# Optimization experiments

Hardware: AMD Instinct MI355X
Metric: run time of the kernel (lower is better)

## Reference

```python
import jax, jax.numpy as jnp
import numpy as np

D = 128      # d_model
H = 8        # n_heads
HD = D // H  # head_dim = 16
E = 256      # n_experts
R = 32       # kv_lora_rank
B, T = 4, 512
EPS = 1e-6


def _dense_init(k, fi, fo):
    s = float(1.0 / np.sqrt(fi))
    return jax.random.uniform(k, (fi, fo), minval=-s, maxval=s, dtype=jnp.float32)


def setup_inputs() -> dict:
    key = jax.random.key(0)
    ks = jax.random.split(key, 16)
    rng = np.random.RandomState(42)
    Q, _ = np.linalg.qr(rng.randn(D, D))
    glim = float(np.sqrt(6.0 / (D + D)))
    return {
        'x': jax.random.normal(ks[0], (B, T, D), dtype=jnp.float32),
        'g1': jnp.ones((D,), jnp.float32),
        'qW': _dense_init(ks[1], D, D), 'qb': jnp.zeros((D,), jnp.float32),
        'kdW': _dense_init(ks[2], D, R), 'kdb': jnp.zeros((R,), jnp.float32),
        'kuW': _dense_init(ks[3], R, 2 * D), 'kub': jnp.zeros((2 * D,), jnp.float32),
        'oW': _dense_init(ks[4], D, D), 'ob': jnp.zeros((D,), jnp.float32),
        'rot': jnp.asarray(Q, jnp.float32),
        'tq_scale': jnp.ones((D,), jnp.float32),
        's1W': _dense_init(ks[5], D, D), 's1b': jnp.zeros((D,), jnp.float32),
        's2W': _dense_init(ks[6], D, D), 's2b': jnp.zeros((D,), jnp.float32),
        'g2': jnp.ones((D,), jnp.float32),
        'gateW': _dense_init(ks[7], D, E), 'gateb': jnp.zeros((E,), jnp.float32),
        'expW': jax.random.uniform(ks[8], (E, D, D), minval=-glim, maxval=glim, dtype=jnp.float32),
        'm1W': _dense_init(ks[9], D, D), 'm1b': jnp.zeros((D,), jnp.float32),
        'm2W': _dense_init(ks[10], D, D), 'm2b': jnp.zeros((D,), jnp.float32),
    }


def _rmsnorm(x, g):
    return g * (x / jnp.sqrt(jnp.mean(x * x, axis=-1, keepdims=True) + EPS))


def _swiglu(x, w1, b1, w2, b2):
    gate = x @ w1 + b1
    return gate * jax.nn.sigmoid(gate) * (x @ w2 + b2)


def _mla(x, qW, qb, kdW, kdb, kuW, kub, oW, ob):
    b, t = x.shape[0], x.shape[1]
    q = (x @ qW + qb).reshape(b, t, H, HD)
    kv = ((x @ kdW + kdb) @ kuW + kub).reshape(b, t, H, 2 * HD)
    k, v = jnp.split(kv, 2, axis=-1)
    q = jax.nn.elu(q) + 1.0
    k = jax.nn.elu(k) + 1.0
    # linear attention: context[b,h,d,e] = sum_t k[b,t,h,d] v[b,t,h,e]
    context = jnp.einsum('bthd,bthe->bhde', k, v)
    out = jnp.einsum('bthd,bhde->bthe', q, context)
    k_sum = jnp.sum(k, axis=1)  # [b,h,d]
    z = 1.0 / (jnp.einsum('bthd,bhd->bth', q, k_sum) + EPS)
    out = out * z[..., None]
    return out.reshape(b, t, D) @ oW + ob


def _turbo_quant(x, rot, scale):
    x = x @ rot
    mag = jnp.sqrt(jnp.mean(x * x, axis=-1, keepdims=True) + EPS)
    phase = x / mag
    qp = jnp.clip(phase * 127.0, -127.0, 127.0) / 127.0
    phase = jax.lax.stop_gradient(qp - phase) + phase  # straight-through
    return phase * mag * scale


def _moe(h, gateW, gateb, expW, m1W, m1b, m2W, m2b):
    gate_scores = jax.nn.softmax(h @ gateW + gateb, axis=-1)  # [B,T,E]
    top_vals, top_idx = jax.lax.top_k(gate_scores, 2)
    top_w = top_vals / (jnp.sum(top_vals, axis=-1, keepdims=True) + EPS)
    # dense all-expert compute as in the original module
    eo = jnp.einsum('btd,edo->bteo', h, expW)  # [B,T,E,D]
    mask = jnp.sum(jax.nn.one_hot(top_idx, E, dtype=h.dtype) * top_w[..., None], axis=2)  # [B,T,E]
    wavg = jnp.einsum('bteo,bte->bto', eo, mask)
    wavg = _swiglu(wavg, m1W, m1b, m2W, m2b)
    diff_sq = jnp.square(eo - wavg[:, :, None, :])
    wvar = jnp.einsum('bteo,bte->bto', diff_sq, mask)
    consensus = jnp.exp(-jnp.mean(wvar, axis=-1))  # [B,T]
    return wavg, consensus


def reference(x, g1, qW, qb, kdW, kdb, kuW, kub, oW, ob, rot, tq_scale,
              s1W, s1b, s2W, s2b, g2, gateW, gateb, expW, m1W, m1b, m2W, m2b):
    attn_out = _turbo_quant(_mla(_rmsnorm(x, g1), qW, qb, kdW, kdb, kuW, kub, oW, ob), rot, tq_scale)
    x = x + _swiglu(attn_out, s1W, s1b, s2W, s2b)
    moe_out, consensus = _moe(_rmsnorm(x, g2), gateW, gateb, expW, m1W, m1b, m2W, m2b)
    return x + moe_out, consensus
```

## Files before the change

### kernel.cpp

```cpp
#include <hip/hip_runtime.h>
#include <math.h>

static constexpr int Dd    = 128;
static constexpr int NH    = 8;
static constexpr int NE    = 256;
static constexpr int RR    = 32;
static constexpr int TT    = 512;
static constexpr int NTOK  = 2048;
static constexpr int SLOTS = 256;
#define EPSF 1e-6f

static constexpr int FK_KV    = 0;
static constexpr int FD_CTX   = 4;
static constexpr int FD_OR    = 8;
static constexpr int FD_ROUTE = 9;
static constexpr int FD_EXP   = 10;
static constexpr int NFLAGS   = 266;

__device__ __forceinline__ float elu1(float v) { return v > 0.f ? v + 1.f : expf(v); }
__device__ __forceinline__ float sigm(float v) { return 1.f / (1.f + expf(-v)); }

__device__ __forceinline__ void flag_add(int* p) {
  __hip_atomic_fetch_add(p, 1, __ATOMIC_RELEASE, __HIP_MEMORY_SCOPE_AGENT);
}
__device__ __forceinline__ void flag_wait(int* p, int tgt) {
  int c = 0;
  while (__hip_atomic_load(p, __ATOMIC_ACQUIRE, __HIP_MEMORY_SCOPE_AGENT) < tgt) {
    __builtin_amdgcn_s_sleep(2);
    if (++c > (1 << 27)) break;
  }
}

struct AParams {
  const float *x, *g1, *qW, *qb, *kdW, *kdb, *kuW, *kub, *oW, *ob, *rot, *tqs;
  const float *s1W, *s1b, *s2W, *s2b, *g2, *gateW, *gateb, *expW;
  const float *m1W, *m1b, *m2W, *m2b;
  float *kvbuf, *ctx, *ksum, *oR, *bR, *h2buf, *ybuf, *out;
  int *cnt, *slottok, *flags;
};

__global__ __launch_bounds__(512, 4) void k_all(AParams P) {
  const int tid = threadIdx.x;
  const int bid = blockIdx.x;
  const int j = tid & 127, g = tid >> 7;
  const int lane = tid & 63;
  const int n0 = bid * 4;
  const int b = bid >> 7;

  __shared__ float sh[64 * 32];
  __shared__ float4 bufA[128], bufB[128];
  __shared__ float4 part[3][128];
  __shared__ float4 gpart[256];
  __shared__ float4 rtmp[2];
  __shared__ float wvS[4][4]; __shared__ int wiS[4][4];
  __shared__ float zS[4][4];
  __shared__ int sE[4][2]; __shared__ int sSlot[4][2]; __shared__ float sWt[4][2];
  __shared__ __align__(16) float hT[128 * 20];
  __shared__ float4 y1T[128], y2T[128], inT[128], sT[128];

  float4* kpart4 = (float4*)hT;
  float4* kdT4   = (float4*)(hT + 1024);

  float xres[4];
  {
    float v[4];
    if (tid < 128) {
#pragma unroll
      for (int t = 0; t < 4; t++) { xres[t] = P.x[(n0 + t) * Dd + j]; v[t] = xres[t] * xres[t]; }
#pragma unroll
      for (int o = 32; o > 0; o >>= 1) {
#pragma unroll
        for (int t = 0; t < 4; t++) v[t] += __shfl_xor(v[t], o, 64);
      }
      if (lane == 0) rtmp[tid >> 6] = make_float4(v[0], v[1], v[2], v[3]);
    }
  }
  __syncthreads();
  if (tid < 128) {
    float g1j = P.g1[j];
#pragma unroll
    for (int t = 0; t < 4; t++) {
      float ss = ((const float*)&rtmp[0])[t] + ((const float*)&rtmp[1])[t];
      ((float*)&bufB[j])[t] = g1j * xres[t] * rsqrtf(ss * (1.f / 128.f) + EPSF);
    }
  }
  __syncthreads();

  {
    float a0 = 0, a1 = 0, a2 = 0, a3 = 0;
    const float* Wp = P.qW + (g * 32) * Dd + j;
#pragma unroll 16
    for (int i = 0; i < 32; i++) {
      float4 h4 = bufB[g * 32 + i];
      float w = Wp[i * Dd];
      a0 += h4.x * w; a1 += h4.y * w; a2 += h4.z * w; a3 += h4.w * w;
    }
    if (g) part[g - 1][j] = make_float4(a0, a1, a2, a3);
    __syncthreads();
    if (g == 0) {
      float4 p0 = part[0][j], p1 = part[1][j], p2 = part[2][j];
      float bb = P.qb[j];
      ((float*)&bufA[j])[0] = elu1(a0 + p0.x + p1.x + p2.x + bb);
      ((float*)&bufA[j])[1] = elu1(a1 + p0.y + p1.y + p2.y + bb);
      ((float*)&bufA[j])[2] = elu1(a2 + p0.z + p1.z + p2.z + bb);
      ((float*)&bufA[j])[3] = elu1(a3 + p0.w + p1.w + p2.w + bb);
    }
    __syncthreads();
  }

  if (tid < 256) {
    int col = tid & 31, ksp = tid >> 5;
    float a0 = 0, a1 = 0, a2 = 0, a3 = 0;
    const float* Wp = P.kdW + (ksp * 16) * RR + col;
#pragma unroll
    for (int i = 0; i < 16; i++) {
      float4 h4 = bufB[ksp * 16 + i];
      float w = Wp[i * RR];
      a0 += h4.x * w; a1 += h4.y * w; a2 += h4.z * w; a3 += h4.w * w;
    }
    kpart4[ksp * 32 + col] = make_float4(a0, a1, a2, a3);
  }
  __syncthreads();
  if (tid < 32) {
    float bb = P.kdb[tid];
    float s0 = bb, s1 = bb, s2 = bb, s3 = bb;
#pragma unroll
    for (int k = 0; k < 8; k++) {
      float4 p = kpart4[k * 32 + tid];
      s0 += p.x; s1 += p.y; s2 += p.z; s3 += p.w;
    }
    kdT4[tid] = make_float4(s0, s1, s2, s3);
  }
  __syncthreads();

  {
    int col = tid & 255, kh = tid >> 8;
    float a0 = 0, a1 = 0, a2 = 0, a3 = 0;
    const float* Wp = P.kuW + (kh * 16) * 256 + col;
#pragma unroll
    for (int r = 0; r < 16; r++) {
      float4 k4 = kdT4[kh * 16 + r];
      float w = Wp[r * 256];
      a0 += k4.x * w; a1 += k4.y * w; a2 += k4.z * w; a3 += k4.w * w;
    }
    if (kh) gpart[col] = make_float4(a0, a1, a2, a3);
    __syncthreads();
    if (!kh) {
      float4 p = gpart[col];
      float bb = P.kub[col];
      bool isk = (col & 31) < 16;
      float v0 = a0 + p.x + bb, v1 = a1 + p.y + bb, v2 = a2 + p.z + bb, v3 = a3 + p.w + bb;
      P.kvbuf[(n0 + 0) * 256 + col] = isk ? elu1(v0) : v0;
      P.kvbuf[(n0 + 1) * 256 + col] = isk ? elu1(v1) : v1;
      P.kvbuf[(n0 + 2) * 256 + col] = isk ? elu1(v2) : v2;
      P.kvbuf[(n0 + 3) * 256 + col] = isk ? elu1(v3) : v3;
    }
  }
  __threadfence();
  __syncthreads();
  if (tid == 0) flag_add(&P.flags[FK_KV + b]);

  if (bid < 32) {
    int idx = bid * 512 + tid;
    int row = idx >> 7, col = idx & 127;
    const float* ow = P.oW + row * 128;
    float acc = 0.f;
#pragma unroll 8
    for (int k = 0; k < 128; k++) acc += ow[k] * P.rot[k * 128 + col];
    P.oR[idx] = acc;
    __threadfence();
    __syncthreads();
    if (tid == 0) flag_add(&P.flags[FD_OR]);
  } else if (bid == 32) {
    if (tid < 128) {
      float acc = 0.f;
#pragma unroll 8
      for (int k = 0; k < 128; k++) acc += P.ob[k] * P.rot[k * 128 + tid];
      P.bR[tid] = acc;
    }
    __threadfence();
    __syncthreads();
    if (tid == 0) flag_add(&P.flags[FD_OR]);
  }

  if (bid < 32) {
    const int bh = bid, bb = bh >> 3, h = bh & 7;
    if (tid == 0) flag_wait(&P.flags[FK_KV + bb], 128);
    __syncthreads();
    __threadfence();
    float acc = 0.f, ks = 0.f;
    const int d = tid >> 4, e = tid & 15;
    for (int c = 0; c < 8; c++) {
      __syncthreads();
#pragma unroll
      for (int r = 0; r < 4; r++) {
        int lin = r * 512 + tid;
        int tok = lin >> 5, off = lin & 31;
        sh[lin] = P.kvbuf[((bb * TT + c * 64 + tok) * 256) + h * 32 + off];
      }
      __syncthreads();
      if (tid < 256) {
#pragma unroll 4
        for (int t = 0; t < 64; t++) {
          float kk = sh[t * 32 + d];
          acc += kk * sh[t * 32 + 16 + e];
          ks += kk;
        }
      }
    }
    if (tid < 256) {
      P.ctx[bh * 256 + d * 16 + e] = acc;
      if (e == 0) P.ksum[bh * 16 + d] = ks;
    }
    __threadfence();
    __syncthreads();
    if (tid == 0) flag_add(&P.flags[FD_CTX + bb]);
  }

  if (tid == 0) flag_wait(&P.flags[FD_CTX + b], 8);
  if (tid == 1) flag_wait(&P.flags[FD_OR], 33);
  __syncthreads();
  __threadfence();

  if (tid < 128) {
    int h = j >> 4, e = j & 15;
    const float* cpt = P.ctx + (b * NH + h) * 256;
    const float* kpt = P.ksum + (b * NH + h) * 16;
    float num[4] = {0, 0, 0, 0}, den[4] = {0, 0, 0, 0};
#pragma unroll
    for (int d = 0; d < 16; d++) {
      float cx = cpt[d * 16 + e], ks = kpt[d];
      float4 q4 = bufA[h * 16 + d];
      num[0] += q4.x * cx; num[1] += q4.y * cx; num[2] += q4.z * cx; num[3] += q4.w * cx;
      den[0] += q4.x * ks; den[1] += q4.y * ks; den[2] += q4.z * ks; den[3] += q4.w * ks;
    }
#pragma unroll
    for (int t = 0; t < 4; t++) ((float*)&bufB[j])[t] = num[t] / (den[t] + EPSF);
  }
  __syncthreads();

  {
    float a0 = 0, a1 = 0, a2 = 0, a3 = 0;
    const float* Wp = P.oR + (g * 32) * Dd + j;
#pragma unroll 16
    for (int i = 0; i < 32; i++) {
      float4 h4 = bufB[g * 32 + i];
      float w = Wp[i * Dd];
      a0 += h4.x * w; a1 += h4.y * w; a2 += h4.z * w; a3 += h4.w * w;
    }
    if (g) part[g - 1][j] = make_float4(a0, a1, a2, a3);
    __syncthreads();
    float tot[4];
    if (g == 0) {
      float4 p0 = part[0][j], p1 = part[1][j], p2 = part[2][j];
      float bb = P.bR[j];
      tot[0] = a0 + p0.x + p1.x + p2.x + bb; tot[1] = a1 + p0.y + p1.y + p2.y + bb;
      tot[2] = a2 + p0.z + p1.z + p2.z + bb; tot[3] = a3 + p0.w + p1.w + p2.w + bb;
      float v[4];
#pragma unroll
      for (int t = 0; t < 4; t++) v[t] = tot[t] * tot[t];
#pragma unroll
      for (int o = 32; o > 0; o >>= 1) {
#pragma unroll
        for (int t = 0; t < 4; t++) v[t] += __shfl_xor(v[t], o, 64);
      }
      if (lane == 0) rtmp[tid >> 6] = make_float4(v[0], v[1], v[2], v[3]);
    }
    __syncthreads();
    if (g == 0) {
      float scj = P.tqs[j];
#pragma unroll
      for (int t = 0; t < 4; t++) {
        float ss = ((const float*)&rtmp[0])[t] + ((const float*)&rtmp[1])[t];
        float mag = sqrtf(ss * (1.f / 128.f) + EPSF);
        float zc = fminf(fmaxf(tot[t], -mag), mag);
        ((float*)&bufA[j])[t] = zc * scj;
      }
    }
    __syncthreads();
  }

  float xn[4] = {0.f, 0.f, 0.f, 0.f};
  {
    float a0 = 0, a1 = 0, a2 = 0, a3 = 0;
    const float* Wp = (g < 2 ? P.s1W : P.s2W) + ((g & 1) * 64) * Dd + j;
#pragma unroll 16
    for (int i = 0; i < 64; i++) {
      float4 h4 = bufA[(g & 1) * 64 + i];
      float w = Wp[i * Dd];
      a0 += h4.x * w; a1 += h4.y * w; a2 += h4.z * w; a3 += h4.w * w;
    }
    if (g) part[g - 1][j] = make_float4(a0, a1, a2, a3);
    __syncthreads();
    if (g == 0) {
      float b1 = P.s1b[j], b2 = P.s2b[j];
      float4 p0 = part[0][j], p1 = part[1][j], p2 = part[2][j];
      float gv[4], uv[4], v[4];
      gv[0] = a0 + p0.x + b1; gv[1] = a1 + p0.y + b1;
      gv[2] = a2 + p0.z + b1; gv[3] = a3 + p0.w + b1;
      uv[0] = p1.x + p2.x + b2; uv[1] = p1.y + p2.y + b2;
      uv[2] = p1.z + p2.z + b2; uv[3] = p1.w + p2.w + b2;
      float g2j = P.g2[j];
#pragma unroll
      for (int t = 0; t < 4; t++) {
        xn[t] = xres[t] + gv[t] * sigm(gv[t]) * uv[t];
        ((float*)&bufB[j])[t] = g2j * xn[t];
        v[t] = xn[t] * xn[t];
      }
#pragma unroll
      for (int o = 32; o > 0; o >>= 1) {
#pragma unroll
        for (int t = 0; t < 4; t++) v[t] += __shfl_xor(v[t], o, 64);
      }
      if (lane == 0) rtmp[tid >> 6] = make_float4(v[0], v[1], v[2], v[3]);
    }
    __syncthreads();
  }

  float val[4]; float r2v[4];
  {
    int col = tid & 255, kh = tid >> 8;
    float a0 = 0, a1 = 0, a2 = 0, a3 = 0;
    const float* Wp = P.gateW + (kh * 64) * NE + col;
#pragma unroll 16
    for (int i = 0; i < 64; i++) {
      float4 h4 = bufB[kh * 64 + i];
      float w = Wp[i * NE];
      a0 += h4.x * w; a1 += h4.y * w; a2 += h4.z * w; a3 += h4.w * w;
    }
    if (kh) gpart[col] = make_float4(a0, a1, a2, a3);
    __syncthreads();
#pragma unroll
    for (int t = 0; t < 4; t++) {
      float ss = ((const float*)&rtmp[0])[t] + ((const float*)&rtmp[1])[t];
      r2v[t] = rsqrtf(ss * (1.f / 128.f) + EPSF);
    }
    if (!kh) {
      float4 p = gpart[col];
      float bb = P.gateb[col];
      val[0] = (a0 + p.x) * r2v[0] + bb; val[1] = (a1 + p.y) * r2v[1] + bb;
      val[2] = (a2 + p.z) * r2v[2] + bb; val[3] = (a3 + p.w) * r2v[3] + bb;
    }
    if (tid < 128) {
#pragma unroll
      for (int t = 0; t < 4; t++)
        P.h2buf[(n0 + t) * Dd + j] = ((const float*)&bufB[j])[t] * r2v[t];
    }
  }
  __syncthreads();

  float m1[4]; int i1[4];
  {
    if (tid < 256) {
      float bv[4]; int bi[4];
#pragma unroll
      for (int t = 0; t < 4; t++) { bv[t] = val[t]; bi[t] = tid; }
#pragma unroll
      for (int o = 32; o > 0; o >>= 1) {
#pragma unroll
        for (int t = 0; t < 4; t++) {
          float wv = __shfl_xor(bv[t], o, 64);
          int wi = __shfl_xor(bi[t], o, 64);
          if (wv > bv[t] || (wv == bv[t] && wi < bi[t])) { bv[t] = wv; bi[t] = wi; }
        }
      }
      if (lane == 0) {
#pragma unroll
        for (int t = 0; t < 4; t++) { wvS[tid >> 6][t] = bv[t]; wiS[tid >> 6][t] = bi[t]; }
      }
    }
    __syncthreads();
    if (tid < 256) {
#pragma unroll
      for (int t = 0; t < 4; t++) {
        m1[t] = wvS[0][t]; i1[t] = wiS[0][t];
#pragma unroll
        for (int w = 1; w < 4; w++) {
          float cv = wvS[w][t]; int ci = wiS[w][t];
          if (cv > m1[t] || (cv == m1[t] && ci < i1[t])) { m1[t] = cv; i1[t] = ci; }
        }
      }
    }
    __syncthreads();
  }
  float m2[4]; int i2[4];
  {
    if (tid < 256) {
      float bv[4]; int bi[4];
#pragma unroll
      for (int t = 0; t < 4; t++) {
        bv[t] = (tid == i1[t]) ? -INFINITY : val[t];
        bi[t] = tid;
      }
#pragma unroll
      for (int o = 32; o > 0; o >>= 1) {
#pragma unroll
        for (int t = 0; t < 4; t++) {
          float wv = __shfl_xor(bv[t], o, 64);
          int wi = __shfl_xor(bi[t], o, 64);
          if (wv > bv[t] || (wv == bv[t] && wi < bi[t])) { bv[t] = wv; bi[t] = wi; }
        }
      }
      if (lane == 0) {
#pragma unroll
        for (int t = 0; t < 4; t++) { wvS[tid >> 6][t] = bv[t]; wiS[tid >> 6][t] = bi[t]; }
      }
    }
    __syncthreads();
    if (tid < 256) {
#pragma unroll
      for (int t = 0; t < 4; t++) {
        m2[t] = wvS[0][t]; i2[t] = wiS[0][t];
#pragma unroll
        for (int w = 1; w < 4; w++) {
          float cv = wvS[w][t]; int ci = wiS[w][t];
          if (cv > m2[t] || (cv == m2[t] && ci < i2[t])) { m2[t] = cv; i2[t] = ci; }
        }
      }
    }
    __syncthreads();
  }
  {
    if (tid < 256) {
      float v[4];
#pragma unroll
      for (int t = 0; t < 4; t++) v[t] = expf(val[t] - m1[t]);
#pragma unroll
      for (int o = 32; o > 0; o >>= 1) {
#pragma unroll
        for (int t = 0; t < 4; t++) v[t] += __shfl_xor(v[t], o, 64);
      }
      if (lane == 0) {
#pragma unroll
        for (int t = 0; t < 4; t++) zS[tid >> 6][t] = v[t];
      }
    }
    __syncthreads();
  }
  if (tid < 4) {
    int t = tid, tok = n0 + t;
    float Z = zS[0][t] + zS[1][t] + zS[2][t] + zS[3][t];
    float p1 = 1.f / Z;
    float p2 = expf(m2[t] - m1[t]) / Z;
    float s = p1 + p2 + EPSF;
    int e1 = i1[t], e2 = i2[t];
    int s1 = atomicAdd(&P.cnt[e1], 1); if (s1 > SLOTS - 1) s1 = SLOTS - 1;
    int s2 = atomicAdd(&P.cnt[e2], 1); if (s2 > SLOTS - 1) s2 = SLOTS - 1;
    int sl1 = e1 * SLOTS + s1, sl2 = e2 * SLOTS + s2;
    P.slottok[sl1] = tok; P.slottok[sl2] = tok;
    sE[t][0] = e1; sE[t][1] = e2;
    sSlot[t][0] = sl1; sSlot[t][1] = sl2;
    sWt[t][0] = p1 / s; sWt[t][1] = p2 / s;
  }

  __threadfence();
  __syncthreads();
  if (tid == 0) {
    flag_add(&P.flags[FD_ROUTE]);
    flag_wait(&P.flags[FD_ROUTE], 512);
  }
  __syncthreads();
  __threadfence();

  {
    const int e = bid >> 1, sub = bid & 1;
    int n = __hip_atomic_load(&P.cnt[e], __ATOMIC_RELAXED, __HIP_MEMORY_SCOPE_AGENT);
    if (n > SLOTS) n = SLOTS;
    const int base = e * SLOTS;
    const float* Wp = P.expW + (size_t)e * Dd * Dd + j;
    for (int t0 = sub * 16; t0 < n; t0 += 32) {
      int m = n - t0; if (m > 16) m = 16;
      __syncthreads();
      for (int tt = g; tt < m; tt += 4) {
        int tok = P.slottok[base + t0 + tt];
        hT[j * 20 + tt] = P.h2buf[tok * Dd + j];
      }
      __syncthreads();
      float acc[4] = {0, 0, 0, 0};
#pragma unroll 8
      for (int i = 0; i < 128; i++) {
        float w = Wp[i * Dd];
        float4 h4 = *(const float4*)&hT[i * 20 + g * 4];
        acc[0] += h4.x * w; acc[1] += h4.y * w; acc[2] += h4.z * w; acc[3] += h4.w * w;
      }
#pragma unroll
      for (int k = 0; k < 4; k++) {
        int tt = g * 4 + k;
        if (tt < m) P.ybuf[(size_t)(base + t0 + tt) * Dd + j] = acc[k];
      }
    }
    __threadfence();
    __syncthreads();
    if (tid == 0) flag_add(&P.flags[FD_EXP + e]);
  }

  if (tid < 8) {
    int t = tid >> 1, sl = tid & 1;
    flag_wait(&P.flags[FD_EXP + sE[t][sl]], 2);
  }
  __syncthreads();
  __threadfence();

  {
    float y1 = P.ybuf[(size_t)sSlot[g][0] * Dd + j];
    float y2 = P.ybuf[(size_t)sSlot[g][1] * Dd + j];
    ((float*)&y1T[j])[g] = y1;
    ((float*)&y2T[j])[g] = y2;
    ((float*)&inT[j])[g] = sWt[g][0] * y1 + sWt[g][1] * y2;
  }
  __syncthreads();

  {
    float a0 = 0, a1 = 0, a2 = 0, a3 = 0;
    const float* Wp = (g < 2 ? P.m1W : P.m2W) + ((g & 1) * 64) * Dd + j;
#pragma unroll 16
    for (int i = 0; i < 64; i++) {
      float4 h4 = inT[(g & 1) * 64 + i];
      float w = Wp[i * Dd];
      a0 += h4.x * w; a1 += h4.y * w; a2 += h4.z * w; a3 += h4.w * w;
    }
    if (g) part[g - 1][j] = make_float4(a0, a1, a2, a3);
    __syncthreads();
    if (g == 0) {
      float b1 = P.m1b[j], b2 = P.m2b[j];
      float4 p0 = part[0][j], p1 = part[1][j], p2 = part[2][j];
      float gv[4], uv[4];
      gv[0] = a0 + p0.x + b1; gv[1] = a1 + p0.y + b1;
      gv[2] = a2 + p0.z + b1; gv[3] = a3 + p0.w + b1;
      uv[0] = p1.x + p2.x + b2; uv[1] = p1.y + p2.y + b2;
      uv[2] = p1.z + p2.z + b2; uv[3] = p1.w + p2.w + b2;
#pragma unroll
      for (int t = 0; t < 4; t++) {
        float sv = gv[t] * sigm(gv[t]) * uv[t];
        ((float*)&sT[j])[t] = sv;
        P.out[(n0 + t) * Dd + j] = xn[t] + sv;
      }
    }
    __syncthreads();
  }

  if (tid < 128) {
    float v[4];
#pragma unroll
    for (int t = 0; t < 4; t++) {
      float sv = ((const float*)&sT[j])[t];
      float d1 = ((const float*)&y1T[j])[t] - sv;
      float d2 = ((const float*)&y2T[j])[t] - sv;
      v[t] = sWt[t][0] * d1 * d1 + sWt[t][1] * d2 * d2;
    }
#pragma unroll
    for (int o = 32; o > 0; o >>= 1) {
#pragma unroll
      for (int t = 0; t < 4; t++) v[t] += __shfl_xor(v[t], o, 64);
    }
    if (lane == 0) rtmp[tid >> 6] = make_float4(v[0], v[1], v[2], v[3]);
  }
  __syncthreads();
  if (tid < 4) {
    float s = ((const float*)&rtmp[0])[tid] + ((const float*)&rtmp[1])[tid];
    P.out[NTOK * Dd + n0 + tid] = expf(-s * (1.f / 128.f));
  }
}

__global__ __launch_bounds__(512) void k_pre_fb(
    const float* __restrict__ x, const float* __restrict__ g1,
    const float* __restrict__ qW, const float* __restrict__ qb,
    const float* __restrict__ kdW, const float* __restrict__ kdb,
    const float* __restrict__ kuW, const float* __restrict__ kub,
    const float* __restrict__ oW, const float* __restrict__ ob,
    const float* __restrict__ rot,
    float* __restrict__ qbuf, float* __restrict__ kvbuf,
    float* __restrict__ ctx, float* __restrict__ ksum,
    int* __restrict__ cnt,
    float* __restrict__ oR, float* __restrict__ bR) {
  const int tid = threadIdx.x;
  const int bid = blockIdx.x;
  const int j = tid & 127, g = tid >> 7;
  const int lane = tid & 63;
  const int n0 = bid * 4;

  __shared__ float4 h1T[128];
  __shared__ float4 part[3][128];
  __shared__ float4 kpart[8][32];
  __shared__ float4 kdT[32];
  __shared__ float4 kupart[256];
  __shared__ float4 rtmp[2];

  if (bid == 0) {
    for (int i = tid; i < 32 * 256; i += 512) ctx[i] = 0.f;
    ksum[tid] = 0.f;
    if (tid < NE) cnt[tid] = 0;
  }

  float xv[4];
  if (tid < 128) {
    float v[4];
#pragma unroll
    for (int t = 0; t < 4; t++) { xv[t] = x[(n0 + t) * Dd + j]; v[t] = xv[t] * xv[t]; }
#pragma unroll
    for (int o = 32; o > 0; o >>= 1) {
#pragma unroll
      for (int t = 0; t < 4; t++) v[t] += __shfl_xor(v[t], o, 64);
    }
    if (lane == 0) rtmp[tid >> 6] = make_float4(v[0], v[1], v[2], v[3]);
  }
  __syncthreads();
  if (tid < 128) {
    float g1j = g1[j];
#pragma unroll
    for (int t = 0; t < 4; t++) {
      float ss = ((const float*)&rtmp[0])[t] + ((const float*)&rtmp[1])[t];
      ((float*)&h1T[j])[t] = g1j * xv[t] * rsqrtf(ss * (1.f / 128.f) + EPSF);
    }
  }
  __syncthreads();

  {
    float a0 = 0, a1 = 0, a2 = 0, a3 = 0;
    const float* Wp = qW + (g * 32) * Dd + j;
#pragma unroll 16
    for (int i = 0; i < 32; i++) {
      float4 h4 = h1T[g * 32 + i];
      float w = Wp[i * Dd];
      a0 += h4.x * w; a1 += h4.y * w; a2 += h4.z * w; a3 += h4.w * w;
    }
    if (g) part[g - 1][j] = make_float4(a0, a1, a2, a3);
    __syncthreads();
    if (g == 0) {
      float4 p0 = part[0][j], p1 = part[1][j], p2 = part[2][j];
      float bb = qb[j];
      qbuf[(n0 + 0) * Dd + j] = elu1(a0 + p0.x + p1.x + p2.x + bb);
      qbuf[(n0 + 1) * Dd + j] = elu1(a1 + p0.y + p1.y + p2.y + bb);
      qbuf[(n0 + 2) * Dd + j] = elu1(a2 + p0.z + p1.z + p2.z + bb);
      qbuf[(n0 + 3) * Dd + j] = elu1(a3 + p0.w + p1.w + p2.w + bb);
    }
    __syncthreads();
  }

  if (tid < 256) {
    int col = tid & 31, ksp = tid >> 5;
    float a0 = 0, a1 = 0, a2 = 0, a3 = 0;
    const float* Wp = kdW + (ksp * 16) * RR + col;
#pragma unroll
    for (int i = 0; i < 16; i++) {
      float4 h4 = h1T[ksp * 16 + i];
      float w = Wp[i * RR];
      a0 += h4.x * w; a1 += h4.y * w; a2 += h4.z * w; a3 += h4.w * w;
    }
    kpart[ksp][col] = make_float4(a0, a1, a2, a3);
  }
  __syncthreads();
  if (tid < 32) {
    float bb = kdb[tid];
    float s0 = bb, s1 = bb, s2 = bb, s3 = bb;
#pragma unroll
    for (int k = 0; k < 8; k++) {
      float4 p = kpart[k][tid];
      s0 += p.x; s1 += p.y; s2 += p.z; s3 += p.w;
    }
    kdT[tid] = make_float4(s0, s1, s2, s3);
  }
  __syncthreads();

  {
    int col = tid & 255, kh = tid >> 8;
    float a0 = 0, a1 = 0, a2 = 0, a3 = 0;
    const float* Wp = kuW + (kh * 16) * 256 + col;
#pragma unroll
    for (int r = 0; r < 16; r++) {
      float4 k4 = kdT[kh * 16 + r];
      float w = Wp[r * 256];
      a0 += k4.x * w; a1 += k4.y * w; a2 += k4.z * w; a3 += k4.w * w;
    }
    if (kh) kupart[col] = make_float4(a0, a1, a2, a3);
    __syncthreads();
    if (!kh) {
      float4 p = kupart[col];
      float bb = kub[col];
      bool isk = (col & 31) < 16;
      float v0 = a0 + p.x + bb, v1 = a1 + p.y + bb, v2 = a2 + p.z + bb, v3 = a3 + p.w + bb;
      kvbuf[(n0 + 0) * 256 + col] = isk ? elu1(v0) : v0;
      kvbuf[(n0 + 1) * 256 + col] = isk ? elu1(v1) : v1;
      kvbuf[(n0 + 2) * 256 + col] = isk ? elu1(v2) : v2;
      kvbuf[(n0 + 3) * 256 + col] = isk ? elu1(v3) : v3;
    }
  }

  if (bid < 32) {
    int idx = bid * 512 + tid;
    int row = idx >> 7, col = idx & 127;
    const float* ow = oW + row * 128;
    float acc = 0.f;
#pragma unroll 8
    for (int k = 0; k < 128; k++) acc += ow[k] * rot[k * 128 + col];
    oR[idx] = acc;
  } else if (bid == 32 && tid < 128) {
    float acc = 0.f;
#pragma unroll 8
    for (int k = 0; k < 128; k++) acc += ob[k] * rot[k * 128 + tid];
    bR[tid] = acc;
  }
}

__global__ __launch_bounds__(256) void k_ctx_fb(const float* __restrict__ kv,
                                                float* __restrict__ ctx,
                                                float* __restrict__ ksum) {
  const int blk = blockIdx.x;
  const int tid = threadIdx.x;
  const int bh = blk >> 3, c = blk & 7;
  const int b = bh >> 3, h = bh & 7;
  const int d = tid >> 4, e = tid & 15;
  __shared__ float sh[64 * 32];
#pragma unroll
  for (int r = 0; r < 8; r++) {
    int lin = r * 256 + tid;
    int tok = lin >> 5, off = lin & 31;
    sh[lin] = kv[((b * TT + c * 64 + tok) * 256) + h * 32 + off];
  }
  __syncthreads();
  float acc = 0.f, ks = 0.f;
#pragma unroll 4
  for (int t = 0; t < 64; t++) {
    float kk = sh[t * 32 + d];
    acc += kk * sh[t * 32 + 16 + e];
    ks += kk;
  }
  atomicAdd(&ctx[bh * 256 + d * 16 + e], acc);
  if (e == 0) atomicAdd(&ksum[bh * 16 + d], ks);
}

__global__ __launch_bounds__(512) void k_mid_fb(
    const float* __restrict__ x, const float* __restrict__ qbuf,
    const float* __restrict__ ctx, const float* __restrict__ ksum,
    const float* __restrict__ oR, const float* __restrict__ bR,
    const float* __restrict__ tqs,
    const float* __restrict__ s1W, const float* __restrict__ s1b,
    const float* __restrict__ s2W, const float* __restrict__ s2b,
    const float* __restrict__ g2, const float* __restrict__ gateW,
    const float* __restrict__ gateb,
    float* __restrict__ xnbuf, float* __restrict__ h2buf,
    float* __restrict__ gw, int* __restrict__ tokslot,
    int* __restrict__ slottok, int* __restrict__ cnt) {
  const int tid = threadIdx.x;
  const int j = tid & 127, g = tid >> 7;
  const int lane = tid & 63;
  const int n0 = blockIdx.x * 4;
  const int b = n0 >> 9;

  __shared__ float4 bufA[128], bufB[128];
  __shared__ float4 part[3][128];
  __shared__ float4 gpart[256];
  __shared__ float4 rtmp[2];
  __shared__ float wvS[4][4]; __shared__ int wiS[4][4];
  __shared__ float zS[4][4];

  float xres[4];
  if (tid < 128) {
#pragma unroll
    for (int t = 0; t < 4; t++) xres[t] = x[(n0 + t) * Dd + j];
  }
  ((float*)&bufA[j])[g] = qbuf[(n0 + g) * Dd + j];
  __syncthreads();

  if (tid < 128) {
    int h = j >> 4, e = j & 15;
    const float* cpt = ctx + (b * NH + h) * 256;
    const float* kpt = ksum + (b * NH + h) * 16;
    float num[4] = {0, 0, 0, 0}, den[4] = {0, 0, 0, 0};
#pragma unroll
    for (int d = 0; d < 16; d++) {
      float cx = cpt[d * 16 + e], ks = kpt[d];
      float4 q4 = bufA[h * 16 + d];
      num[0] += q4.x * cx; num[1] += q4.y * cx; num[2] += q4.z * cx; num[3] += q4.w * cx;
      den[0] += q4.x * ks; den[1] += q4.y * ks; den[2] += q4.z * ks; den[3] += q4.w * ks;
    }
#pragma unroll
    for (int t = 0; t < 4; t++) ((float*)&bufB[j])[t] = num[t] / (den[t] + EPSF);
  }
  __syncthreads();

  {
    float a0 = 0, a1 = 0, a2 = 0, a3 = 0;
    const float* Wp = oR + (g * 32) * Dd + j;
#pragma unroll 16
    for (int i = 0; i < 32; i++) {
      float4 h4 = bufB[g * 32 + i];
      float w = Wp[i * Dd];
      a0 += h4.x * w; a1 += h4.y * w; a2 += h4.z * w; a3 += h4.w * w;
    }
    if (g) part[g - 1][j] = make_float4(a0, a1, a2, a3);
    __syncthreads();
    float tot[4];
    if (g == 0) {
      float4 p0 = part[0][j], p1 = part[1][j], p2 = part[2][j];
      float bb = bR[j];
      tot[0] = a0 + p0.x + p1.x + p2.x + bb; tot[1] = a1 + p0.y + p1.y + p2.y + bb;
      tot[2] = a2 + p0.z + p1.z + p2.z + bb; tot[3] = a3 + p0.w + p1.w + p2.w + bb;
      float v[4];
#pragma unroll
      for (int t = 0; t < 4; t++) v[t] = tot[t] * tot[t];
#pragma unroll
      for (int o = 32; o > 0; o >>= 1) {
#pragma unroll
        for (int t = 0; t < 4; t++) v[t] += __shfl_xor(v[t], o, 64);
      }
      if (lane == 0) rtmp[tid >> 6] = make_float4(v[0], v[1], v[2], v[3]);
    }
    __syncthreads();
    if (g == 0) {
      float scj = tqs[j];
#pragma unroll
      for (int t = 0; t < 4; t++) {
        float ss = ((const float*)&rtmp[0])[t] + ((const float*)&rtmp[1])[t];
        float mag = sqrtf(ss * (1.f / 128.f) + EPSF);
        float zc = fminf(fmaxf(tot[t], -mag), mag);
        ((float*)&bufA[j])[t] = zc * scj;
      }
    }
    __syncthreads();
  }

  {
    float a0 = 0, a1 = 0, a2 = 0, a3 = 0;
    const float* Wp = (g < 2 ? s1W : s2W) + ((g & 1) * 64) * Dd + j;
#pragma unroll 16
    for (int i = 0; i < 64; i++) {
      float4 h4 = bufA[(g & 1) * 64 + i];
      float w = Wp[i * Dd];
      a0 += h4.x * w; a1 += h4.y * w; a2 += h4.z * w; a3 += h4.w * w;
    }
    if (g) part[g - 1][j] = make_float4(a0, a1, a2, a3);
    __syncthreads();
    if (g == 0) {
      float b1 = s1b[j], b2 = s2b[j];
      float4 p0 = part[0][j], p1 = part[1][j], p2 = part[2][j];
      float gv[4], uv[4], xn[4], v[4];
      gv[0] = a0 + p0.x + b1; gv[1] = a1 + p0.y + b1;
      gv[2] = a2 + p0.z + b1; gv[3] = a3 + p0.w + b1;
      uv[0] = p1.x + p2.x + b2; uv[1] = p1.y + p2.y + b2;
      uv[2] = p1.z + p2.z + b2; uv[3] = p1.w + p2.w + b2;
      float g2j = g2[j];
#pragma unroll
      for (int t = 0; t < 4; t++) {
        xn[t] = xres[t] + gv[t] * sigm(gv[t]) * uv[t];
        xnbuf[(n0 + t) * Dd + j] = xn[t];
        ((float*)&bufB[j])[t] = g2j * xn[t];
        v[t] = xn[t] * xn[t];
      }
#pragma unroll
      for (int o = 32; o > 0; o >>= 1) {
#pragma unroll
        for (int t = 0; t < 4; t++) v[t] += __shfl_xor(v[t], o, 64);
      }
      if (lane == 0) rtmp[tid >> 6] = make_float4(v[0], v[1], v[2], v[3]);
    }
    __syncthreads();
  }

  float val[4];
  float r2[4];
  {
    int col = tid & 255, kh = tid >> 8;
    float a0 = 0, a1 = 0, a2 = 0, a3 = 0;
    const float* Wp = gateW + (kh * 64) * NE + col;
#pragma unroll 16
    for (int i = 0; i < 64; i++) {
      float4 h4 = bufB[kh * 64 + i];
      float w = Wp[i * NE];
      a0 += h4.x * w; a1 += h4.y * w; a2 += h4.z * w; a3 += h4.w * w;
    }
    if (kh) gpart[col] = make_float4(a0, a1, a2, a3);
    __syncthreads();
#pragma unroll
    for (int t = 0; t < 4; t++) {
      float ss = ((const float*)&rtmp[0])[t] + ((const float*)&rtmp[1])[t];
      r2[t] = rsqrtf(ss * (1.f / 128.f) + EPSF);
    }
    if (!kh) {
      float4 p = gpart[col];
      float bb = gateb[col];
      val[0] = (a0 + p.x) * r2[0] + bb; val[1] = (a1 + p.y) * r2[1] + bb;
      val[2] = (a2 + p.z) * r2[2] + bb; val[3] = (a3 + p.w) * r2[3] + bb;
    }
    if (tid < 128) {
#pragma unroll
      for (int t = 0; t < 4; t++)
        h2buf[(n0 + t) * Dd + j] = ((const float*)&bufB[j])[t] * r2[t];
    }
  }
  __syncthreads();

  float m1[4]; int i1[4];
  {
    if (tid < 256) {
      float bv[4]; int bi[4];
#pragma unroll
      for (int t = 0; t < 4; t++) { bv[t] = val[t]; bi[t] = tid; }
#pragma unroll
      for (int o = 32; o > 0; o >>= 1) {
#pragma unroll
        for (int t = 0; t < 4; t++) {
          float wv = __shfl_xor(bv[t], o, 64);
          int wi = __shfl_xor(bi[t], o, 64);
          if (wv > bv[t] || (wv == bv[t] && wi < bi[t])) { bv[t] = wv; bi[t] = wi; }
        }
      }
      if (lane == 0) {
#pragma unroll
        for (int t = 0; t < 4; t++) { wvS[tid >> 6][t] = bv[t]; wiS[tid >> 6][t] = bi[t]; }
      }
    }
    __syncthreads();
    if (tid < 256) {
#pragma unroll
      for (int t = 0; t < 4; t++) {
        m1[t] = wvS[0][t]; i1[t] = wiS[0][t];
#pragma unroll
        for (int w = 1; w < 4; w++) {
          float cv = wvS[w][t]; int ci = wiS[w][t];
          if (cv > m1[t] || (cv == m1[t] && ci < i1[t])) { m1[t] = cv; i1[t] = ci; }
        }
      }
    }
    __syncthreads();
  }
  float m2[4]; int i2[4];
  {
    if (tid < 256) {
      float bv[4]; int bi[4];
#pragma unroll
      for (int t = 0; t < 4; t++) {
        bv[t] = (tid == i1[t]) ? -INFINITY : val[t];
        bi[t] = tid;
      }
#pragma unroll
      for (int o = 32; o > 0; o >>= 1) {
#pragma unroll
        for (int t = 0; t < 4; t++) {
          float wv = __shfl_xor(bv[t], o, 64);
          int wi = __shfl_xor(bi[t], o, 64);
          if (wv > bv[t] || (wv == bv[t] && wi < bi[t])) { bv[t] = wv; bi[t] = wi; }
        }
      }
      if (lane == 0) {
#pragma unroll
        for (int t = 0; t < 4; t++) { wvS[tid >> 6][t] = bv[t]; wiS[tid >> 6][t] = bi[t]; }
      }
    }
    __syncthreads();
    if (tid < 256) {
#pragma unroll
      for (int t = 0; t < 4; t++) {
        m2[t] = wvS[0][t]; i2[t] = wiS[0][t];
#pragma unroll
        for (int w = 1; w < 4; w++) {
          float cv = wvS[w][t]; int ci = wiS[w][t];
          if (cv > m2[t] || (cv == m2[t] && ci < i2[t])) { m2[t] = cv; i2[t] = ci; }
        }
      }
    }
    __syncthreads();
  }
  {
    if (tid < 256) {
      float v[4];
#pragma unroll
      for (int t = 0; t < 4; t++) v[t] = expf(val[t] - m1[t]);
#pragma unroll
      for (int o = 32; o > 0; o >>= 1) {
#pragma unroll
        for (int t = 0; t < 4; t++) v[t] += __shfl_xor(v[t], o, 64);
      }
      if (lane == 0) {
#pragma unroll
        for (int t = 0; t < 4; t++) zS[tid >> 6][t] = v[t];
      }
    }
    __syncthreads();
  }
  if (tid < 4) {
    int t = tid, tok = n0 + t;
    float Z = zS[0][t] + zS[1][t] + zS[2][t] + zS[3][t];
    float p1 = 1.f / Z;
    float p2 = expf(m2[t] - m1[t]) / Z;
    float s = p1 + p2 + EPSF;
    int e1 = i1[t], e2 = i2[t];
    int s1 = atomicAdd(&cnt[e1], 1); if (s1 > SLOTS - 1) s1 = SLOTS - 1;
    int s2 = atomicAdd(&cnt[e2], 1); if (s2 > SLOTS - 1) s2 = SLOTS - 1;
    int sl1 = e1 * SLOTS + s1, sl2 = e2 * SLOTS + s2;
    slottok[sl1] = tok; slottok[sl2] = tok;
    tokslot[tok * 2] = sl1; tokslot[tok * 2 + 1] = sl2;
    gw[tok * 2] = p1 / s; gw[tok * 2 + 1] = p2 / s;
  }
}

__global__ __launch_bounds__(512) void k_exp_fb(const float* __restrict__ h2buf,
                                                const int* __restrict__ slottok,
                                                const int* __restrict__ cnt,
                                                const float* __restrict__ expW,
                                                float* __restrict__ ybuf) {
  const int e = blockIdx.x >> 1, sub = blockIdx.x & 1;
  int n = cnt[e]; if (n > SLOTS) n = SLOTS;
  const int base = e * SLOTS;
  const int tid = threadIdx.x;
  const int j = tid & 127, g = tid >> 7;
  __shared__ __align__(16) float hT[128 * 20];
  const float* Wp = expW + (size_t)e * Dd * Dd + j;
  for (int t0 = sub * 16; t0 < n; t0 += 32) {
    int m = n - t0; if (m > 16) m = 16;
    __syncthreads();
    for (int tt = g; tt < m; tt += 4) {
      int tok = slottok[base + t0 + tt];
      hT[j * 20 + tt] = h2buf[tok * Dd + j];
    }
    __syncthreads();
    float acc[4] = {0, 0, 0, 0};
#pragma unroll 8
    for (int i = 0; i < 128; i++) {
      float w = Wp[i * Dd];
      float4 h4 = *(const float4*)&hT[i * 20 + g * 4];
      acc[0] += h4.x * w; acc[1] += h4.y * w; acc[2] += h4.z * w; acc[3] += h4.w * w;
    }
#pragma unroll
    for (int k = 0; k < 4; k++) {
      int tt = g * 4 + k;
      if (tt < m) ybuf[(size_t)(base + t0 + tt) * Dd + j] = acc[k];
    }
  }
}

__global__ __launch_bounds__(512) void k_post_fb(
    const float* __restrict__ xnbuf, const float* __restrict__ ybuf,
    const int* __restrict__ tokslot, const float* __restrict__ gw,
    const float* __restrict__ m1W, const float* __restrict__ m1b,
    const float* __restrict__ m2W, const float* __restrict__ m2b,
    float* __restrict__ out) {
  const int tid = threadIdx.x;
  const int j = tid & 127, g = tid >> 7;
  const int lane = tid & 63;
  const int n0 = blockIdx.x * 4;

  __shared__ float4 y1T[128], y2T[128], inT[128], sT[128];
  __shared__ float4 part[3][128];
  __shared__ float4 rtmp[2];
  __shared__ int sSlot[4][2];
  __shared__ float sWt[4][2];

  if (tid < 4) {
    sSlot[tid][0] = tokslot[(n0 + tid) * 2];
    sSlot[tid][1] = tokslot[(n0 + tid) * 2 + 1];
    sWt[tid][0] = gw[(n0 + tid) * 2];
    sWt[tid][1] = gw[(n0 + tid) * 2 + 1];
  }
  __syncthreads();

  {
    float y1 = ybuf[(size_t)sSlot[g][0] * Dd + j];
    float y2 = ybuf[(size_t)sSlot[g][1] * Dd + j];
    ((float*)&y1T[j])[g] = y1;
    ((float*)&y2T[j])[g] = y2;
    ((float*)&inT[j])[g] = sWt[g][0] * y1 + sWt[g][1] * y2;
  }
  __syncthreads();

  {
    float a0 = 0, a1 = 0, a2 = 0, a3 = 0;
    const float* Wp = (g < 2 ? m1W : m2W) + ((g & 1) * 64) * Dd + j;
#pragma unroll 16
    for (int i = 0; i < 64; i++) {
      float4 h4 = inT[(g & 1) * 64 + i];
      float w = Wp[i * Dd];
      a0 += h4.x * w; a1 += h4.y * w; a2 += h4.z * w; a3 += h4.w * w;
    }
    if (g) part[g - 1][j] = make_float4(a0, a1, a2, a3);
    __syncthreads();
    if (g == 0) {
      float b1 = m1b[j], b2 = m2b[j];
      float4 p0 = part[0][j], p1 = part[1][j], p2 = part[2][j];
      float gv[4], uv[4];
      gv[0] = a0 + p0.x + b1; gv[1] = a1 + p0.y + b1;
      gv[2] = a2 + p0.z + b1; gv[3] = a3 + p0.w + b1;
      uv[0] = p1.x + p2.x + b2; uv[1] = p1.y + p2.y + b2;
      uv[2] = p1.z + p2.z + b2; uv[3] = p1.w + p2.w + b2;
#pragma unroll
      for (int t = 0; t < 4; t++) {
        float sv = gv[t] * sigm(gv[t]) * uv[t];
        ((float*)&sT[j])[t] = sv;
        out[(n0 + t) * Dd + j] = xnbuf[(n0 + t) * Dd + j] + sv;
      }
    }
    __syncthreads();
  }

  if (tid < 128) {
    float v[4];
#pragma unroll
    for (int t = 0; t < 4; t++) {
      float sv = ((const float*)&sT[j])[t];
      float d1 = ((const float*)&y1T[j])[t] - sv;
      float d2 = ((const float*)&y2T[j])[t] - sv;
      v[t] = sWt[t][0] * d1 * d1 + sWt[t][1] * d2 * d2;
    }
#pragma unroll
    for (int o = 32; o > 0; o >>= 1) {
#pragma unroll
      for (int t = 0; t < 4; t++) v[t] += __shfl_xor(v[t], o, 64);
    }
    if (lane == 0) rtmp[tid >> 6] = make_float4(v[0], v[1], v[2], v[3]);
  }
  __syncthreads();
  if (tid < 4) {
    float s = ((const float*)&rtmp[0])[tid] + ((const float*)&rtmp[1])[tid];
    out[NTOK * Dd + n0 + tid] = expf(-s * (1.f / 128.f));
  }
}

extern "C" void kernel_launch(void* const* d_in, const int* in_sizes, int n_in,
                              void* d_out, int out_size, void* d_ws, size_t ws_size,
                              hipStream_t stream) {
  const float* x   = (const float*)d_in[0];
  const float* g1  = (const float*)d_in[1];
  const float* qW  = (const float*)d_in[2];
  const float* qb  = (const float*)d_in[3];
  const float* kdW = (const float*)d_in[4];
  const float* kdb = (const float*)d_in[5];
  const float* kuW = (const float*)d_in[6];
  const float* kub = (const float*)d_in[7];
  const float* oW  = (const float*)d_in[8];
  const float* ob  = (const float*)d_in[9];
  const float* rot = (const float*)d_in[10];
  const float* tqs = (const float*)d_in[11];
  const float* s1W = (const float*)d_in[12];
  const float* s1b = (const float*)d_in[13];
  const float* s2W = (const float*)d_in[14];
  const float* s2b = (const float*)d_in[15];
  const float* g2  = (const float*)d_in[16];
  const float* gW  = (const float*)d_in[17];
  const float* gb  = (const float*)d_in[18];
  const float* eW  = (const float*)d_in[19];
  const float* m1W = (const float*)d_in[20];
  const float* m1b = (const float*)d_in[21];
  const float* m2W = (const float*)d_in[22];
  const float* m2b = (const float*)d_in[23];
  float* out = (float*)d_out;
  float* ws  = (float*)d_ws;

  float* ctx     = ws;
  float* ksum    = ws + 8192;
  float* oR      = ws + 8704;
  float* bR      = ws + 25088;
  float* kvbuf   = ws + 25216;
  float* h2buf   = ws + 549504;
  float* ybuf    = ws + 811648;
  int*   slottok = (int*)(ws + 9200256);
  int*   cnt     = (int*)(ws + 9265792);
  int*   flags   = (int*)(ws + 9266048);
  float* qbuf    = ws + 9266560;
  float* xnbuf   = ws + 9528704;
  float* gw      = ws + 9790848;
  int*   tokslot = (int*)(ws + 9794944);

  hipMemsetAsync(cnt, 0, (256 + 512) * sizeof(int), stream);

  AParams p;
  p.x = x; p.g1 = g1; p.qW = qW; p.qb = qb; p.kdW = kdW; p.kdb = kdb;
  p.kuW = kuW; p.kub = kub; p.oW = oW; p.ob = ob; p.rot = rot; p.tqs = tqs;
  p.s1W = s1W; p.s1b = s1b; p.s2W = s2W; p.s2b = s2b; p.g2 = g2;
  p.gateW = gW; p.gateb = gb; p.expW = eW;
  p.m1W = m1W; p.m1b = m1b; p.m2W = m2W; p.m2b = m2b;
  p.kvbuf = kvbuf; p.ctx = ctx; p.ksum = ksum; p.oR = oR; p.bR = bR;
  p.h2buf = h2buf; p.ybuf = ybuf; p.out = out;
  p.cnt = cnt; p.slottok = slottok; p.flags = flags;

  void* args[] = {(void*)&p};
  hipError_t err = hipErrorUnknown;
  int nb = 0;
  if (hipOccupancyMaxActiveBlocksPerMultiprocessor(
          &nb, reinterpret_cast<const void*>(&k_all), 512, 0) == hipSuccess &&
      nb >= 2) {
    err = hipLaunchCooperativeKernel((void*)k_all, dim3(NTOK / 4), dim3(512),
                                     args, 0u, stream);
  }
  if (err == hipSuccess) return;

  k_pre_fb<<<NTOK / 4, 512, 0, stream>>>(x, g1, qW, qb, kdW, kdb, kuW, kub,
                                         oW, ob, rot, qbuf, kvbuf, ctx, ksum,
                                         cnt, oR, bR);
  k_ctx_fb<<<256, 256, 0, stream>>>(kvbuf, ctx, ksum);
  k_mid_fb<<<NTOK / 4, 512, 0, stream>>>(x, qbuf, ctx, ksum, oR, bR, tqs,
                                         s1W, s1b, s2W, s2b, g2, gW, gb,
                                         xnbuf, h2buf, gw, tokslot, slottok, cnt);
  k_exp_fb<<<NE * 2, 512, 0, stream>>>(h2buf, slottok, cnt, eW, ybuf);
  k_post_fb<<<NTOK / 4, 512, 0, stream>>>(xnbuf, ybuf, tokslot, gw,
                                          m1W, m1b, m2W, m2b, out);
}
```

Baseline: 163.2 us.

## Split linear-attention context reduction across 256 blocks and use hierarchical route barrier

The key-value context reduction is spread over 256 blocks (one per batch-head and 64-token chunk) instead of 32, with partial sums combined by float atomicAdd into a zero-initialised ctx/ksum buffer. Each chunk now waits only on the finer-grained per-chunk kv flag rather than the whole batch. The route grid barrier is made two-level (8 group counters feeding a root counter) to reduce contention on one atomic. The workspace is reordered so one memset clears ctx, ksum, counts and flags, at the cost of atomic accumulation order nondeterminism.

```diff
diff --git a/kernel.cpp b/kernel.cpp
--- a/kernel.cpp
+++ b/kernel.cpp
@@ -11,11 +11,11 @@
 #define EPSF 1e-6f
 
 static constexpr int FK_KV    = 0;
-static constexpr int FD_CTX   = 4;
-static constexpr int FD_OR    = 8;
-static constexpr int FD_ROUTE = 9;
-static constexpr int FD_EXP   = 10;
-static constexpr int NFLAGS   = 266;
+static constexpr int FD_CTX   = 32;
+static constexpr int FD_OR    = 36;
+static constexpr int FD_RG    = 37;
+static constexpr int FD_ROOT  = 45;
+static constexpr int FD_EXP   = 46;
 
 __device__ __forceinline__ float elu1(float v) { return v > 0.f ? v + 1.f : expf(v); }
 __device__ __forceinline__ float sigm(float v) { return 1.f / (1.f + expf(-v)); }
@@ -158,10 +158,38 @@
   }
   __threadfence();
   __syncthreads();
-  if (tid == 0) flag_add(&P.flags[FK_KV + b]);
-
-  if (bid < 32) {
-    int idx = bid * 512 + tid;
+  if (tid == 0) flag_add(&P.flags[FK_KV + b * 8 + ((bid & 127) >> 4)]);
+
+  if (bid < 256) {
+    const int bh = bid >> 3, c = bid & 7;
+    const int bb = bh >> 3, h = bh & 7;
+    if (tid == 0) flag_wait(&P.flags[FK_KV + bb * 8 + c], 16);
+    __syncthreads();
+    __threadfence();
+#pragma unroll
+    for (int r = 0; r < 4; r++) {
+      int lin = r * 512 + tid;
+      int tok = lin >> 5, off = lin & 31;
+      sh[lin] = P.kvbuf[((bb * TT + c * 64 + tok) * 256) + h * 32 + off];
+    }
+    __syncthreads();
+    if (tid < 256) {
+      const int d = tid >> 4, e = tid & 15;
+      float acc = 0.f, ks = 0.f;
+#pragma unroll 4
+      for (int t = 0; t < 64; t++) {
+        float kk = sh[t * 32 + d];
+        acc += kk * sh[t * 32 + 16 + e];
+        ks += kk;
+      }
+      atomicAdd(&P.ctx[bh * 256 + d * 16 + e], acc);
+      if (e == 0) atomicAdd(&P.ksum[bh * 16 + d], ks);
+    }
+    __threadfence();
+    __syncthreads();
+    if (tid == 0) flag_add(&P.flags[FD_CTX + bb]);
+  } else if (bid < 288) {
+    int idx = (bid - 256) * 512 + tid;
     int row = idx >> 7, col = idx & 127;
     const float* ow = P.oW + row * 128;
     float acc = 0.f;
@@ -171,7 +199,7 @@
     __threadfence();
     __syncthreads();
     if (tid == 0) flag_add(&P.flags[FD_OR]);
-  } else if (bid == 32) {
+  } else if (bid == 288) {
     if (tid < 128) {
       float acc = 0.f;
 #pragma unroll 8
@@ -183,41 +211,7 @@
     if (tid == 0) flag_add(&P.flags[FD_OR]);
   }
 
-  if (bid < 32) {
-    const int bh = bid, bb = bh >> 3, h = bh & 7;
-    if (tid == 0) flag_wait(&P.flags[FK_KV + bb], 128);
-    __syncthreads();
-    __threadfence();
-    float acc = 0.f, ks = 0.f;
-    const int d = tid >> 4, e = tid & 15;
-    for (int c = 0; c < 8; c++) {
-      __syncthreads();
-#pragma unroll
-      for (int r = 0; r < 4; r++) {
-        int lin = r * 512 + tid;
-        int tok = lin >> 5, off = lin & 31;
-        sh[lin] = P.kvbuf[((bb * TT + c * 64 + tok) * 256) + h * 32 + off];
-      }
-      __syncthreads();
-      if (tid < 256) {
-#pragma unroll 4
-        for (int t = 0; t < 64; t++) {
-          float kk = sh[t * 32 + d];
-          acc += kk * sh[t * 32 + 16 + e];
-          ks += kk;
-        }
-      }
-    }
-    if (tid < 256) {
-      P.ctx[bh * 256 + d * 16 + e] = acc;
-      if (e == 0) P.ksum[bh * 16 + d] = ks;
-    }
-    __threadfence();
-    __syncthreads();
-    if (tid == 0) flag_add(&P.flags[FD_CTX + bb]);
-  }
-
-  if (tid == 0) flag_wait(&P.flags[FD_CTX + b], 8);
+  if (tid == 0) flag_wait(&P.flags[FD_CTX + b], 64);
   if (tid == 1) flag_wait(&P.flags[FD_OR], 33);
   __syncthreads();
   __threadfence();
@@ -456,8 +450,11 @@
   __threadfence();
   __syncthreads();
   if (tid == 0) {
-    flag_add(&P.flags[FD_ROUTE]);
-    flag_wait(&P.flags[FD_ROUTE], 512);
+    int grp = bid >> 6;
+    int prev = __hip_atomic_fetch_add(&P.flags[FD_RG + grp], 1,
+                                      __ATOMIC_ACQ_REL, __HIP_MEMORY_SCOPE_AGENT);
+    if (prev == 63) flag_add(&P.flags[FD_ROOT]);
+    flag_wait(&P.flags[FD_ROOT], 8);
   }
   __syncthreads();
   __threadfence();
@@ -1147,20 +1144,20 @@
 
   float* ctx     = ws;
   float* ksum    = ws + 8192;
-  float* oR      = ws + 8704;
-  float* bR      = ws + 25088;
-  float* kvbuf   = ws + 25216;
-  float* h2buf   = ws + 549504;
-  float* ybuf    = ws + 811648;
-  int*   slottok = (int*)(ws + 9200256);
-  int*   cnt     = (int*)(ws + 9265792);
-  int*   flags   = (int*)(ws + 9266048);
+  int*   cnt     = (int*)(ws + 8704);
+  int*   flags   = (int*)(ws + 8960);
+  float* oR      = ws + 9472;
+  float* bR      = ws + 25856;
+  float* kvbuf   = ws + 25984;
+  float* h2buf   = ws + 550272;
+  float* ybuf    = ws + 812416;
+  int*   slottok = (int*)(ws + 9201024);
   float* qbuf    = ws + 9266560;
   float* xnbuf   = ws + 9528704;
   float* gw      = ws + 9790848;
   int*   tokslot = (int*)(ws + 9794944);
 
-  hipMemsetAsync(cnt, 0, (256 + 512) * sizeof(int), stream);
+  hipMemsetAsync(ws, 0, (8192 + 512 + 256 + 512) * sizeof(float), stream);
 
   AParams p;
   p.x = x; p.g1 = g1; p.qW = qW; p.qb = qb; p.kdW = kdW; p.kdb = kdb;
```

New measurement: 163.3 us. No clear change (+0.1%).
